# Kernel tuning notes

Measured on AMD Instinct MI355X. Metric: run time of the kernel, lower is better.

The kernel has to match this reference:

```python
import jax, jax.numpy as jnp
import numpy as np

N_NODES = 100000
N_EDGES = 1600000
NFEAT = 128
NHID = 128
NCLASS = 16
NUM_GRAPHS = 64
EPS = 1e-5


def layer_norm(x, g, b):
    mu = jnp.mean(x, axis=-1, keepdims=True)
    var = jnp.mean((x - mu) ** 2, axis=-1, keepdims=True)
    return (x - mu) * jax.lax.rsqrt(var + EPS) * g + b


def gcn_conv(x, W, b, src, dst, ew, n_nodes):
    # PyG GCNConv: h = x @ W^T; add self loops (weight 1); sym-normalize; scatter-add; + bias
    h = x @ W.T                                   # [N, out]
    loop = jnp.arange(n_nodes, dtype=src.dtype)
    src2 = jnp.concatenate([src, loop])
    dst2 = jnp.concatenate([dst, loop])
    ew2 = jnp.concatenate([ew, jnp.ones((n_nodes,), dtype=ew.dtype)])
    deg = jax.ops.segment_sum(ew2, dst2, num_segments=n_nodes)
    dinv = jnp.where(deg > 0, jax.lax.rsqrt(jnp.where(deg > 0, deg, 1.0)), 0.0)
    norm = dinv[src2] * ew2 * dinv[dst2]          # [E+N]
    msg = h[src2] * norm[:, None]                 # gather + scale
    agg = jax.ops.segment_sum(msg, dst2, num_segments=n_nodes)
    return agg + b


def setup_inputs() -> dict:
    key = jax.random.key(0)
    ks = jax.random.split(key, 12)
    kaiming = lambda k, shape: jax.random.normal(k, shape, dtype=jnp.float32) * np.sqrt(2.0 / shape[1])
    ln = lambda k, d: (1.0 + 0.02 * jax.random.normal(k, (d,), dtype=jnp.float32),
                       0.02 * jax.random.normal(jax.random.fold_in(k, 1), (d,), dtype=jnp.float32))
    ln0_g, ln0_b = ln(ks[0], NFEAT)
    ln1_g, ln1_b = ln(ks[1], NHID)
    ln2_g, ln2_b = ln(ks[2], NHID)
    # batch vector: sorted graph ids so each graph is a contiguous node block
    batch = jnp.sort(jax.random.randint(ks[3], (N_NODES,), 0, NUM_GRAPHS)).astype(jnp.int64)
    return {
        "x": jax.random.normal(ks[4], (N_NODES, NFEAT), dtype=jnp.float32),
        "edge_index": jax.random.randint(ks[5], (2, N_EDGES), 0, N_NODES).astype(jnp.int64),
        "batch": batch,
        "edge_weight": jnp.ones((N_EDGES,), dtype=jnp.float32),
        "ln0_g": ln0_g, "ln0_b": ln0_b,
        "W1": kaiming(ks[6], (NHID, NFEAT)), "b1": jnp.zeros((NHID,), jnp.float32),
        "ln1_g": ln1_g, "ln1_b": ln1_b,
        "W2": kaiming(ks[7], (NHID, NHID)), "b2": jnp.zeros((NHID,), jnp.float32),
        "ln2_g": ln2_g, "ln2_b": ln2_b,
        "Wc": kaiming(ks[8], (NCLASS, NHID)), "bc": jnp.zeros((NCLASS,), jnp.float32),
    }


def reference(x, edge_index, batch, edge_weight,
              ln0_g, ln0_b, W1, b1, ln1_g, ln1_b,
              W2, b2, ln2_g, ln2_b, Wc, bc):
    src, dst = edge_index[0], edge_index[1]
    h = layer_norm(x, ln0_g, ln0_b)                       # layer_norm_first
    h = gcn_conv(h, W1, b1, src, dst, edge_weight, N_NODES)
    h = jax.nn.relu(layer_norm(h, ln1_g, ln1_b))          # dropout is identity in eval
    h = gcn_conv(h, W2, b2, src, dst, edge_weight, N_NODES)
    h = jax.nn.relu(layer_norm(h, ln2_g, ln2_b))
    pooled = jax.ops.segment_sum(h, batch, num_segments=NUM_GRAPHS)  # global_add_pool
    logits = pooled @ Wc.T + bc
    return jax.nn.log_softmax(logits, axis=1)
```

## Files before the change

### kernel.cpp

```cpp
#include <hip/hip_runtime.h>
#include <hip/hip_bf16.h>
#include <math.h>

#define N_NODES 100000
#define NFEAT 128
#define NCLASS 16
#define NUM_GRAPHS 64
#define LN_EPS 1e-5f
#define PAD 40
#define BSHIFT 7
#define NBKT 782
#define BCAP 2560
#define EPB 4096

typedef unsigned int uint;
typedef unsigned short ushort;
typedef unsigned char uchar;
typedef short bf16x8 __attribute__((ext_vector_type(8)));
typedef float f32x4 __attribute__((ext_vector_type(4)));
typedef float f32x2 __attribute__((ext_vector_type(2)));

__device__ __forceinline__ float wave_sum64(float v) {
#pragma unroll
    for (int m = 32; m >= 1; m >>= 1) v += __shfl_xor(v, m, 64);
    return v;
}

__device__ __forceinline__ float bf_lo(uint u) { return __uint_as_float(u << 16); }
__device__ __forceinline__ float bf_hi(uint u) { return __uint_as_float(u & 0xffff0000u); }
__device__ __forceinline__ ushort f2bf(float f) {
    uint u = __float_as_uint(f);
    uint r = 0x7fffu + ((u >> 16) & 1u);
    return (ushort)((u + r) >> 16);
}
__device__ __forceinline__ uint pack2bf(float x, float y) {
    return ((uint)f2bf(y) << 16) | (uint)f2bf(x);
}
__device__ __forceinline__ uint pk15(float f) {
    uint u = __float_as_uint(f);
    uint r = 0xFFFFu + ((u >> 17) & 1u);
    return (u + r) >> 17;
}
__device__ __forceinline__ float up15(uint w) {
    return __uint_as_float(w << 17);
}

#if __has_builtin(__builtin_amdgcn_cvt_pk_f32_fp8)
__device__ __forceinline__ f32x2 fp8lo(uint u) {
    return __builtin_amdgcn_cvt_pk_f32_fp8((int)u, false);
}
__device__ __forceinline__ f32x2 fp8hi(uint u) {
    return __builtin_amdgcn_cvt_pk_f32_fp8((int)u, true);
}
#else
__device__ __forceinline__ float fp8_one(uint b) {
    uint em = b & 0x7fu;
    float v;
    if (em >= 0x08u) v = __uint_as_float((((em >> 3) + 120u) << 23) | ((em & 7u) << 20));
    else v = (float)em * (1.0f / 512.0f);
    return (b & 0x80u) ? -v : v;
}
__device__ __forceinline__ f32x2 fp8lo(uint u) {
    f32x2 r;
    r[0] = fp8_one(u & 0xffu);
    r[1] = fp8_one((u >> 8) & 0xffu);
    return r;
}
__device__ __forceinline__ f32x2 fp8hi(uint u) { return fp8lo(u >> 16); }
#endif

#if __has_builtin(__builtin_amdgcn_cvt_pk_fp8_f32)
__device__ __forceinline__ uint f2fp8(float f) {
    return (uint)__builtin_amdgcn_cvt_pk_fp8_f32(f, f, 0, false) & 0xffu;
}
#else
__device__ __forceinline__ uint f2fp8(float f) {
    uint u = __float_as_uint(f);
    uint s = (u >> 24) & 0x80u;
    uint mag = u & 0x7fffffffu;
    if (mag >= 0x43E80000u) return s | 0x7Eu;
    if (mag < 0x3C800000u) {
        uint q = (uint)(__uint_as_float(mag) * 512.0f + 0.5f);
        return s | q;
    }
    uint r = 0x7FFFFu + ((mag >> 20) & 1u);
    mag += r;
    uint e = (mag >> 23) - 120u;
    uint m = (mag >> 20) & 7u;
    if (e > 15u) return s | 0x7Eu;
    return s | (e << 3) | m;
}
#endif

__global__ void k_setup(int* __restrict__ gfill, float* __restrict__ pooled,
                        const float* __restrict__ W1, const float* __restrict__ W2,
                        ushort* __restrict__ Wf) {
    int i = blockIdx.x * 256 + threadIdx.x;
    if (i < NBKT) gfill[i] = 0;
    if (i < NUM_GRAPHS * NFEAT) pooled[i] = 0.0f;
    if (i < 2 * NFEAT * NFEAT) {
        int f = i & 16383;
        const float* W = (i < NFEAT * NFEAT) ? W1 : W2;
        int e = f & 7, lane = (f >> 3) & 63, c = (f >> 9) & 3, t = f >> 11;
        int m = lane & 15, q = lane >> 4;
        Wf[i] = f2bf(W[(t * 16 + m) * NFEAT + c * 32 + q * 8 + e]);
    }
}

__global__ __launch_bounds__(256) void k_bin(const int* __restrict__ dst,
                                             const int* __restrict__ src,
                                             const float* __restrict__ ew,
                                             int* __restrict__ gfill,
                                             uint2* __restrict__ binned, int E) {
    __shared__ int lcnt[NBKT];
    __shared__ int lbase[NBKT];
    int t = threadIdx.x;
    int e0 = blockIdx.x * EPB;
    for (int i = t; i < NBKT; i += 256) lcnt[i] = 0;
    __syncthreads();
    int myb[16], myd[16];
#pragma unroll
    for (int i = 0; i < 16; ++i) {
        int e = e0 + i * 256 + t;
        int b = -1, d = 0;
        if (e < E) {
            d = dst[e];
            b = d >> BSHIFT;
            atomicAdd(&lcnt[b], 1);
        }
        myb[i] = b;
        myd[i] = d;
    }
    __syncthreads();
    for (int i = t; i < NBKT; i += 256) {
        int c = lcnt[i];
        lbase[i] = (c > 0) ? atomicAdd(&gfill[i], c) : 0;
        lcnt[i] = 0;
    }
    __syncthreads();
#pragma unroll
    for (int i = 0; i < 16; ++i) {
        int e = e0 + i * 256 + t;
        if (e >= E) continue;
        int b = myb[i];
        int ofs = lbase[b] + atomicAdd(&lcnt[b], 1);
        if (ofs < BCAP) {
            uint s = (uint)src[e];
            binned[(size_t)b * BCAP + ofs] =
                make_uint2(((uint)(myd[i] & 127) << 17) | s, __float_as_uint(ew[e]));
        }
    }
}

__global__ __launch_bounds__(256) void k_build(const uint2* __restrict__ binned,
                                               const int* __restrict__ gfill,
                                               uint* __restrict__ rowcsr,
                                               int* __restrict__ cnt,
                                               float* __restrict__ dinv, int n) {
    __shared__ uint lcsr[128 * 41];
    __shared__ int lc[128];
    int b = blockIdx.x, t = threadIdx.x;
    int node0 = b << BSHIFT;
    for (int i = t; i < 128 * 41; i += 256) lcsr[i] = 0;
    if (t < 128) lc[t] = 0;
    __syncthreads();
    int c = gfill[b];
    if (c > BCAP) c = BCAP;
    const uint2* rec = binned + (size_t)b * BCAP;
    for (int i = t; i < c; i += 256) {
        uint2 r = rec[i];
        int nl = (int)(r.x >> 17);
        int slot = atomicAdd(&lc[nl], 1);
        if (slot < PAD)
            lcsr[nl * 41 + slot] = ((r.x & 0x1FFFFu) << 15) | pk15(__uint_as_float(r.y));
    }
    __syncthreads();
    int nvalid = n - node0;
    if (nvalid > 128) nvalid = 128;
    if (nvalid <= 0) return;
    size_t gbase = (size_t)node0 * PAD;
    int wtot = nvalid * PAD;
    for (int i = t; i < wtot; i += 256) {
        int nl = i / PAD, sl = i - nl * PAD;
        rowcsr[gbase + i] = lcsr[nl * 41 + sl];
    }
    if (t < nvalid) {
        int cc = lc[t];
        if (cc > PAD) cc = PAD;
        float s = 0.0f;
        for (int r = 0; r < cc; ++r) s += up15(lcsr[t * 41 + r]);
        cnt[node0 + t] = cc;
        dinv[node0 + t] = rsqrtf(1.0f + s);
    }
}

__global__ __launch_bounds__(256) void k_gemm_ln0(const float* __restrict__ X,
                                                  const ushort* __restrict__ Wf,
                                                  const float* __restrict__ dinv,
                                                  const float* __restrict__ lg,
                                                  const float* __restrict__ lb,
                                                  uchar* __restrict__ C, int nrows) {
    int tid = threadIdx.x;
    int wave = tid >> 6, lane = tid & 63;
    int row0 = blockIdx.x * 64 + wave * 16;
    int m = lane & 15, q = lane >> 4;
    int ra = row0 + m;
    float xv[32];
    if (ra < nrows) {
#pragma unroll
        for (int c = 0; c < 4; ++c) {
            float4 p0 = *(const float4*)(X + (size_t)ra * NFEAT + c * 32 + q * 8);
            float4 p1 = *(const float4*)(X + (size_t)ra * NFEAT + c * 32 + q * 8 + 4);
            xv[c * 8 + 0] = p0.x; xv[c * 8 + 1] = p0.y; xv[c * 8 + 2] = p0.z; xv[c * 8 + 3] = p0.w;
            xv[c * 8 + 4] = p1.x; xv[c * 8 + 5] = p1.y; xv[c * 8 + 6] = p1.z; xv[c * 8 + 7] = p1.w;
        }
    } else {
#pragma unroll
        for (int i = 0; i < 32; ++i) xv[i] = 0.0f;
    }
    float s = 0.0f;
#pragma unroll
    for (int i = 0; i < 32; ++i) s += xv[i];
    s += __shfl_xor(s, 16, 64);
    s += __shfl_xor(s, 32, 64);
    float mean = s * (1.0f / NFEAT);
    float v = 0.0f;
#pragma unroll
    for (int i = 0; i < 32; ++i) { float d = xv[i] - mean; v += d * d; }
    v += __shfl_xor(v, 16, 64);
    v += __shfl_xor(v, 32, 64);
    float rs = rsqrtf(v * (1.0f / NFEAT) + LN_EPS);

    bf16x8 a[4];
#pragma unroll
    for (int c = 0; c < 4; ++c) {
        float4 g0 = *(const float4*)(lg + c * 32 + q * 8);
        float4 g1 = *(const float4*)(lg + c * 32 + q * 8 + 4);
        float4 b0 = *(const float4*)(lb + c * 32 + q * 8);
        float4 b1 = *(const float4*)(lb + c * 32 + q * 8 + 4);
        float gv[8] = {g0.x, g0.y, g0.z, g0.w, g1.x, g1.y, g1.z, g1.w};
        float bv[8] = {b0.x, b0.y, b0.z, b0.w, b1.x, b1.y, b1.z, b1.w};
        uint tmp[4];
#pragma unroll
        for (int t2 = 0; t2 < 4; ++t2) {
            float e0 = (xv[c * 8 + 2 * t2] - mean) * rs * gv[2 * t2] + bv[2 * t2];
            float e1 = (xv[c * 8 + 2 * t2 + 1] - mean) * rs * gv[2 * t2 + 1] + bv[2 * t2 + 1];
            tmp[t2] = pack2bf(e0, e1);
        }
        a[c] = *(bf16x8*)tmp;
    }

    int orow[4];
    float sd[4];
#pragma unroll
    for (int r = 0; r < 4; ++r) {
        orow[r] = row0 + q * 4 + r;
        sd[r] = (orow[r] < nrows) ? dinv[orow[r]] : 0.0f;
    }
#pragma unroll
    for (int t = 0; t < 8; ++t) {
        const ushort* bp = Wf + ((t * 4 * 64 + lane) << 3);
        f32x4 acc = {0.0f, 0.0f, 0.0f, 0.0f};
        acc = __builtin_amdgcn_mfma_f32_16x16x32_bf16(a[0], *(const bf16x8*)(bp), acc, 0, 0, 0);
        acc = __builtin_amdgcn_mfma_f32_16x16x32_bf16(a[1], *(const bf16x8*)(bp + 512), acc, 0, 0, 0);
        acc = __builtin_amdgcn_mfma_f32_16x16x32_bf16(a[2], *(const bf16x8*)(bp + 1024), acc, 0, 0, 0);
        acc = __builtin_amdgcn_mfma_f32_16x16x32_bf16(a[3], *(const bf16x8*)(bp + 1536), acc, 0, 0, 0);
#pragma unroll
        for (int r = 0; r < 4; ++r) {
            if (orow[r] < nrows)
                C[(size_t)orow[r] * NFEAT + t * 16 + m] = (uchar)f2fp8(acc[r] * sd[r]);
        }
    }
}

__global__ __launch_bounds__(256) void k_gemm_mfma(const ushort* __restrict__ A,
                                                   const ushort* __restrict__ Wf,
                                                   const float* __restrict__ dinv,
                                                   uchar* __restrict__ C, int nrows) {
    int tid = threadIdx.x;
    int wave = tid >> 6, lane = tid & 63;
    int row0 = blockIdx.x * 64 + wave * 16;
    int m = lane & 15, q = lane >> 4;
    int ra = row0 + m;
    bf16x8 a0 = {0,0,0,0,0,0,0,0}, a1 = a0, a2 = a0, a3 = a0;
    if (ra < nrows) {
        const ushort* p = A + (size_t)ra * NFEAT + q * 8;
        a0 = *(const bf16x8*)(p);
        a1 = *(const bf16x8*)(p + 32);
        a2 = *(const bf16x8*)(p + 64);
        a3 = *(const bf16x8*)(p + 96);
    }
    int orow[4];
    float sd[4];
#pragma unroll
    for (int r = 0; r < 4; ++r) {
        orow[r] = row0 + q * 4 + r;
        sd[r] = (orow[r] < nrows) ? dinv[orow[r]] : 0.0f;
    }
#pragma unroll
    for (int t = 0; t < 8; ++t) {
        const ushort* bp = Wf + ((t * 4 * 64 + lane) << 3);
        f32x4 acc = {0.0f, 0.0f, 0.0f, 0.0f};
        acc = __builtin_amdgcn_mfma_f32_16x16x32_bf16(a0, *(const bf16x8*)(bp), acc, 0, 0, 0);
        acc = __builtin_amdgcn_mfma_f32_16x16x32_bf16(a1, *(const bf16x8*)(bp + 512), acc, 0, 0, 0);
        acc = __builtin_amdgcn_mfma_f32_16x16x32_bf16(a2, *(const bf16x8*)(bp + 1024), acc, 0, 0, 0);
        acc = __builtin_amdgcn_mfma_f32_16x16x32_bf16(a3, *(const bf16x8*)(bp + 1536), acc, 0, 0, 0);
#pragma unroll
        for (int r = 0; r < 4; ++r) {
            if (orow[r] < nrows)
                C[(size_t)orow[r] * NFEAT + t * 16 + m] = (uchar)f2fp8(acc[r] * sd[r]);
        }
    }
}

__global__ __launch_bounds__(256) void k_agg_ln(const uchar* __restrict__ T,
                                                const uint* __restrict__ rowcsr,
                                                const int* __restrict__ cnt,
                                                const float* __restrict__ dinv,
                                                const float* __restrict__ bias,
                                                const float* __restrict__ lng,
                                                const float* __restrict__ lnb,
                                                ushort* __restrict__ out, int n) {
    int wid = blockIdx.x * 4 + (threadIdx.x >> 6);
    int lane = threadIdx.x & 63;
    int half = lane >> 5;
    int l32 = lane & 31;
    int node = wid * 2 + half;
    bool valid = node < n;
    int nodec = valid ? node : 0;

    const uint* Tw = (const uint*)T;
    int c = 0;
    float di = 0.0f;
    if (valid) {
        c = cnt[node];
        di = dinv[node];
    }
    if (c > PAD) c = PAD;
    uint su = Tw[(size_t)nodec * 32 + l32];
    f32x2 s01 = fp8lo(su), s23 = fp8hi(su);
    float a0 = s01[0], a1 = s01[1], a2 = s23[0], a3 = s23[1];

    int cother = __shfl_xor(c, 32, 64);
    int cmax = (c > cother) ? c : cother;
    int rc = (cmax + 7) & ~7;
    const uint* mp = rowcsr + (size_t)nodec * PAD;

    int j = 0;
    for (; j + 16 <= rc; j += 16) {
        uint mw[16];
#pragma unroll
        for (int k = 0; k < 16; k += 4) {
            uint4 m0 = *(const uint4*)(mp + j + k);
            mw[k] = m0.x; mw[k + 1] = m0.y; mw[k + 2] = m0.z; mw[k + 3] = m0.w;
        }
        uint uu[16];
#pragma unroll
        for (int k = 0; k < 16; ++k)
            uu[k] = Tw[(size_t)(mw[k] >> 15) * 32 + l32];
#pragma unroll
        for (int k = 0; k < 16; ++k) {
            float w = up15(mw[k]);
            f32x2 v01 = fp8lo(uu[k]);
            f32x2 v23 = fp8hi(uu[k]);
            a0 = fmaf(v01[0], w, a0);
            a1 = fmaf(v01[1], w, a1);
            a2 = fmaf(v23[0], w, a2);
            a3 = fmaf(v23[1], w, a3);
        }
    }
    for (; j < rc; j += 8) {
        uint4 m0 = *(const uint4*)(mp + j);
        uint4 m1 = *(const uint4*)(mp + j + 4);
        uint mw[8];
        mw[0] = m0.x; mw[1] = m0.y; mw[2] = m0.z; mw[3] = m0.w;
        mw[4] = m1.x; mw[5] = m1.y; mw[6] = m1.z; mw[7] = m1.w;
        uint uu[8];
#pragma unroll
        for (int k = 0; k < 8; ++k)
            uu[k] = Tw[(size_t)(mw[k] >> 15) * 32 + l32];
#pragma unroll
        for (int k = 0; k < 8; ++k) {
            float w = up15(mw[k]);
            f32x2 v01 = fp8lo(uu[k]);
            f32x2 v23 = fp8hi(uu[k]);
            a0 = fmaf(v01[0], w, a0);
            a1 = fmaf(v01[1], w, a1);
            a2 = fmaf(v23[0], w, a2);
            a3 = fmaf(v23[1], w, a3);
        }
    }

    float4 bb = *(const float4*)(bias + 4 * l32);
    float p0 = fmaf(di, a0, bb.x);
    float p1 = fmaf(di, a1, bb.y);
    float p2 = fmaf(di, a2, bb.z);
    float p3 = fmaf(di, a3, bb.w);
    float s = p0 + p1 + p2 + p3;
#pragma unroll
    for (int m = 16; m >= 1; m >>= 1) s += __shfl_xor(s, m, 64);
    float mean = s * (1.0f / NFEAT);
    float d0 = p0 - mean, d1 = p1 - mean, d2 = p2 - mean, d3 = p3 - mean;
    float v = d0 * d0 + d1 * d1 + d2 * d2 + d3 * d3;
#pragma unroll
    for (int m = 16; m >= 1; m >>= 1) v += __shfl_xor(v, m, 64);
    float rs = rsqrtf(v * (1.0f / NFEAT) + LN_EPS);
    float4 gg = *(const float4*)(lng + 4 * l32);
    float4 lbv = *(const float4*)(lnb + 4 * l32);
    float o0 = fmaxf(d0 * rs * gg.x + lbv.x, 0.0f);
    float o1 = fmaxf(d1 * rs * gg.y + lbv.y, 0.0f);
    float o2 = fmaxf(d2 * rs * gg.z + lbv.z, 0.0f);
    float o3 = fmaxf(d3 * rs * gg.w + lbv.w, 0.0f);
    if (valid) {
        uint w0 = pack2bf(o0, o1);
        uint w1 = pack2bf(o2, o3);
        *(uint2*)(out + (size_t)node * NFEAT + 4 * l32) = make_uint2(w0, w1);
    }
}

__global__ __launch_bounds__(256) void k_pool(const ushort* __restrict__ in,
                                              const int* __restrict__ batch,
                                              float* __restrict__ pooled, int n) {
    int wave = blockIdx.x * 4 + (threadIdx.x >> 6);
    int row0 = wave * 16;
    if (row0 >= n) return;
    int lane = threadIdx.x & 63;
    int end = row0 + 16;
    if (end > n) end = n;
    float accx = 0.0f, accy = 0.0f;
    int cur = batch[row0];
    for (int r = row0; r < end; ++r) {
        int g = batch[r];
        if (g != cur) {
            unsafeAtomicAdd(&pooled[cur * NFEAT + 2 * lane], accx);
            unsafeAtomicAdd(&pooled[cur * NFEAT + 2 * lane + 1], accy);
            accx = 0.0f; accy = 0.0f;
            cur = g;
        }
        uint u = *(const uint*)(in + (size_t)r * NFEAT + 2 * lane);
        accx += bf_lo(u);
        accy += bf_hi(u);
    }
    unsafeAtomicAdd(&pooled[cur * NFEAT + 2 * lane], accx);
    unsafeAtomicAdd(&pooled[cur * NFEAT + 2 * lane + 1], accy);
}

__global__ void k_final(const float* __restrict__ pooled, const float* __restrict__ Wc,
                        const float* __restrict__ bc, float* __restrict__ out) {
    __shared__ float p[128];
    __shared__ float lg[NCLASS];
    int g = blockIdx.x, t = threadIdx.x;
    p[t] = pooled[g * 128 + t];
    __syncthreads();
    if (t < NCLASS) {
        float s = bc[t];
        for (int k = 0; k < 128; ++k) s = fmaf(p[k], Wc[t * 128 + k], s);
        lg[t] = s;
    }
    __syncthreads();
    if (t == 0) {
        float m = -1e30f;
        for (int j = 0; j < NCLASS; ++j) m = fmaxf(m, lg[j]);
        float sum = 0.0f;
        for (int j = 0; j < NCLASS; ++j) sum += expf(lg[j] - m);
        float l = logf(sum);
        for (int j = 0; j < NCLASS; ++j) out[g * NCLASS + j] = lg[j] - m - l;
    }
}

extern "C" void kernel_launch(void* const* d_in, const int* in_sizes, int n_in,
                              void* d_out, int out_size, void* d_ws, size_t ws_size,
                              hipStream_t stream) {
    const float* x    = (const float*)d_in[0];
    const int*   ei   = (const int*)d_in[1];
    const int*   batch= (const int*)d_in[2];
    const float* ew   = (const float*)d_in[3];
    const float* ln0g = (const float*)d_in[4];
    const float* ln0b = (const float*)d_in[5];
    const float* W1   = (const float*)d_in[6];
    const float* b1   = (const float*)d_in[7];
    const float* ln1g = (const float*)d_in[8];
    const float* ln1b = (const float*)d_in[9];
    const float* W2   = (const float*)d_in[10];
    const float* b2   = (const float*)d_in[11];
    const float* ln2g = (const float*)d_in[12];
    const float* ln2b = (const float*)d_in[13];
    const float* Wc   = (const float*)d_in[14];
    const float* bc   = (const float*)d_in[15];
    float* out = (float*)d_out;

    int E = in_sizes[1] / 2;
    const int* srcp = ei;
    const int* dstp = ei + E;

    ushort* A     = (ushort*)d_ws;
    ushort* B     = A + (size_t)N_NODES * NFEAT;
    uint*  rowcsr = (uint*)(B + (size_t)N_NODES * NFEAT);
    uint2* binned = (uint2*)(rowcsr + (size_t)N_NODES * PAD);
    float* dinv   = (float*)(binned + (size_t)NBKT * BCAP);
    float* pooled = dinv + N_NODES;
    int*   gfill  = (int*)(pooled + NUM_GRAPHS * NFEAT);
    int*   cnt    = gfill + NBKT;
    ushort* W1f   = (ushort*)(cnt + N_NODES);
    ushort* W2f   = W1f + NFEAT * NFEAT;
    uchar* B8     = (uchar*)B;

    dim3 blk(256);
    int gN = (N_NODES + 255) / 256;
    int gW = ((N_NODES + 1) / 2 + 3) / 4;
    int gG = (N_NODES + 63) / 64;
    int gB = (E + EPB - 1) / EPB;

    k_setup<<<gN, blk, 0, stream>>>(gfill, pooled, W1, W2, W1f);
    k_bin<<<gB, blk, 0, stream>>>(dstp, srcp, ew, gfill, binned, E);
    k_build<<<NBKT, blk, 0, stream>>>(binned, gfill, rowcsr, cnt, dinv, N_NODES);

    k_gemm_ln0<<<gG, blk, 0, stream>>>(x, W1f, dinv, ln0g, ln0b, B8, N_NODES);
    k_agg_ln<<<gW, blk, 0, stream>>>(B8, rowcsr, cnt, dinv, b1, ln1g, ln1b, A, N_NODES);
    k_gemm_mfma<<<gG, blk, 0, stream>>>(A, W2f, dinv, B8, N_NODES);
    k_agg_ln<<<gW, blk, 0, stream>>>(B8, rowcsr, cnt, dinv, b2, ln2g, ln2b, A, N_NODES);
    k_pool<<<(N_NODES + 63) / 64, blk, 0, stream>>>(A, batch, pooled, N_NODES);
    k_final<<<NUM_GRAPHS, dim3(128), 0, stream>>>(pooled, Wc, bc, out);
}
```

Baseline: 292.9 us.

## Build padded CSR directly with global atomics instead of two-pass bucketing

Replaces the bucket-binning plus shared-memory CSR build with a direct scatter. Each edge takes a slot in its destination row through a global atomic counter and writes straight into the zeroed padded row array. A small pass then sums the weights per row for dinv and clamps the counts. This removes the intermediate binned buffer and its extra round trip through memory. In exchange it adds a full zeroing pass over the row array and 1.6M scattered global atomics with uncoalesced writes.

```diff
diff --git a/kernel.cpp b/kernel.cpp
--- a/kernel.cpp
+++ b/kernel.cpp
@@ -8,10 +8,6 @@
 #define NUM_GRAPHS 64
 #define LN_EPS 1e-5f
 #define PAD 40
-#define BSHIFT 7
-#define NBKT 782
-#define BCAP 2560
-#define EPB 4096
 
 typedef unsigned int uint;
 typedef unsigned short ushort;
@@ -19,12 +15,6 @@
 typedef short bf16x8 __attribute__((ext_vector_type(8)));
 typedef float f32x4 __attribute__((ext_vector_type(4)));
 typedef float f32x2 __attribute__((ext_vector_type(2)));
-
-__device__ __forceinline__ float wave_sum64(float v) {
-#pragma unroll
-    for (int m = 32; m >= 1; m >>= 1) v += __shfl_xor(v, m, 64);
-    return v;
-}
 
 __device__ __forceinline__ float bf_lo(uint u) { return __uint_as_float(u << 16); }
 __device__ __forceinline__ float bf_hi(uint u) { return __uint_as_float(u & 0xffff0000u); }
@@ -92,11 +82,15 @@
 }
 #endif
 
-__global__ void k_setup(int* __restrict__ gfill, float* __restrict__ pooled,
-                        const float* __restrict__ W1, const float* __restrict__ W2,
-                        ushort* __restrict__ Wf) {
+__global__ __launch_bounds__(256) void k_zero(uint4* __restrict__ rowcsr4,
+                                              int* __restrict__ cnt,
+                                              float* __restrict__ pooled,
+                                              const float* __restrict__ W1,
+                                              const float* __restrict__ W2,
+                                              ushort* __restrict__ Wf) {
     int i = blockIdx.x * 256 + threadIdx.x;
-    if (i < NBKT) gfill[i] = 0;
+    if (i < (N_NODES * PAD) / 4) rowcsr4[i] = make_uint4(0, 0, 0, 0);
+    if (i < N_NODES) cnt[i] = 0;
     if (i < NUM_GRAPHS * NFEAT) pooled[i] = 0.0f;
     if (i < 2 * NFEAT * NFEAT) {
         int f = i & 16383;
@@ -107,91 +101,54 @@
     }
 }
 
-__global__ __launch_bounds__(256) void k_bin(const int* __restrict__ dst,
-                                             const int* __restrict__ src,
-                                             const float* __restrict__ ew,
-                                             int* __restrict__ gfill,
-                                             uint2* __restrict__ binned, int E) {
-    __shared__ int lcnt[NBKT];
-    __shared__ int lbase[NBKT];
-    int t = threadIdx.x;
-    int e0 = blockIdx.x * EPB;
-    for (int i = t; i < NBKT; i += 256) lcnt[i] = 0;
-    __syncthreads();
-    int myb[16], myd[16];
-#pragma unroll
-    for (int i = 0; i < 16; ++i) {
-        int e = e0 + i * 256 + t;
-        int b = -1, d = 0;
-        if (e < E) {
-            d = dst[e];
-            b = d >> BSHIFT;
-            atomicAdd(&lcnt[b], 1);
-        }
-        myb[i] = b;
-        myd[i] = d;
-    }
-    __syncthreads();
-    for (int i = t; i < NBKT; i += 256) {
-        int c = lcnt[i];
-        lbase[i] = (c > 0) ? atomicAdd(&gfill[i], c) : 0;
-        lcnt[i] = 0;
-    }
-    __syncthreads();
-#pragma unroll
-    for (int i = 0; i < 16; ++i) {
-        int e = e0 + i * 256 + t;
-        if (e >= E) continue;
-        int b = myb[i];
-        int ofs = lbase[b] + atomicAdd(&lcnt[b], 1);
-        if (ofs < BCAP) {
-            uint s = (uint)src[e];
-            binned[(size_t)b * BCAP + ofs] =
-                make_uint2(((uint)(myd[i] & 127) << 17) | s, __float_as_uint(ew[e]));
-        }
-    }
-}
-
-__global__ __launch_bounds__(256) void k_build(const uint2* __restrict__ binned,
-                                               const int* __restrict__ gfill,
-                                               uint* __restrict__ rowcsr,
-                                               int* __restrict__ cnt,
-                                               float* __restrict__ dinv, int n) {
-    __shared__ uint lcsr[128 * 41];
-    __shared__ int lc[128];
-    int b = blockIdx.x, t = threadIdx.x;
-    int node0 = b << BSHIFT;
-    for (int i = t; i < 128 * 41; i += 256) lcsr[i] = 0;
-    if (t < 128) lc[t] = 0;
-    __syncthreads();
-    int c = gfill[b];
-    if (c > BCAP) c = BCAP;
-    const uint2* rec = binned + (size_t)b * BCAP;
-    for (int i = t; i < c; i += 256) {
-        uint2 r = rec[i];
-        int nl = (int)(r.x >> 17);
-        int slot = atomicAdd(&lc[nl], 1);
-        if (slot < PAD)
-            lcsr[nl * 41 + slot] = ((r.x & 0x1FFFFu) << 15) | pk15(__uint_as_float(r.y));
-    }
-    __syncthreads();
-    int nvalid = n - node0;
-    if (nvalid > 128) nvalid = 128;
-    if (nvalid <= 0) return;
-    size_t gbase = (size_t)node0 * PAD;
-    int wtot = nvalid * PAD;
-    for (int i = t; i < wtot; i += 256) {
-        int nl = i / PAD, sl = i - nl * PAD;
-        rowcsr[gbase + i] = lcsr[nl * 41 + sl];
-    }
-    if (t < nvalid) {
-        int cc = lc[t];
-        if (cc > PAD) cc = PAD;
-        float s = 0.0f;
-        for (int r = 0; r < cc; ++r) s += up15(lcsr[t * 41 + r]);
-        cnt[node0 + t] = cc;
-        dinv[node0 + t] = rsqrtf(1.0f + s);
-    }
+__global__ __launch_bounds__(256) void k_direct(const int* __restrict__ dst,
+                                                const int* __restrict__ src,
+                                                const float* __restrict__ ew,
+                                                int* __restrict__ cnt,
+                                                uint* __restrict__ rowcsr, int E) {
+    int e0 = (blockIdx.x * 256 + threadIdx.x) * 4;
+    if (e0 >= E) return;
+    if (e0 + 4 <= E) {
+        int4 d4 = *(const int4*)(dst + e0);
+        int4 s4 = *(const int4*)(src + e0);
+        float4 w4 = *(const float4*)(ew + e0);
+        int dd[4] = {d4.x, d4.y, d4.z, d4.w};
+        int ss[4] = {s4.x, s4.y, s4.z, s4.w};
+        float ww[4] = {w4.x, w4.y, w4.z, w4.w};
+        int slot[4];
+#pragma unroll
+        for (int k = 0; k < 4; ++k) slot[k] = atomicAdd(&cnt[dd[k]], 1);
+#pragma unroll
+        for (int k = 0; k < 4; ++k) {
+            if (slot[k] < PAD)
+                rowcsr[(size_t)dd[k] * PAD + slot[k]] = ((uint)ss[k] << 15) | pk15(ww[k]);
+        }
+    } else {
+        for (int e = e0; e < E; ++e) {
+            int d = dst[e];
+            int slot = atomicAdd(&cnt[d], 1);
+            if (slot < PAD)
+                rowcsr[(size_t)d * PAD + slot] = ((uint)src[e] << 15) | pk15(ew[e]);
+        }
+    }
+}
+
+__global__ __launch_bounds__(256) void k_fix(const uint* __restrict__ rowcsr,
+                                             int* __restrict__ cnt,
+                                             float* __restrict__ dinv, int n) {
+    int i = blockIdx.x * 256 + threadIdx.x;
+    if (i >= n) return;
+    const uint4* p = (const uint4*)(rowcsr + (size_t)i * PAD);
+    float s = 0.0f;
+#pragma unroll
+    for (int r = 0; r < PAD / 4; ++r) {
+        uint4 v = p[r];
+        s += up15(v.x) + up15(v.y) + up15(v.z) + up15(v.w);
+    }
+    int cc = cnt[i];
+    if (cc > PAD) cnt[i] = PAD;
+    (void)cc;
+    dinv[i] = rsqrtf(1.0f + s);
 }
 
 __global__ __launch_bounds__(256) void k_gemm_ln0(const float* __restrict__ X,
@@ -496,24 +453,23 @@
     ushort* A     = (ushort*)d_ws;
     ushort* B     = A + (size_t)N_NODES * NFEAT;
     uint*  rowcsr = (uint*)(B + (size_t)N_NODES * NFEAT);
-    uint2* binned = (uint2*)(rowcsr + (size_t)N_NODES * PAD);
-    float* dinv   = (float*)(binned + (size_t)NBKT * BCAP);
+    float* dinv   = (float*)(rowcsr + (size_t)N_NODES * PAD);
     float* pooled = dinv + N_NODES;
-    int*   gfill  = (int*)(pooled + NUM_GRAPHS * NFEAT);
-    int*   cnt    = gfill + NBKT;
+    int*   cnt    = (int*)(pooled + NUM_GRAPHS * NFEAT);
     ushort* W1f   = (ushort*)(cnt + N_NODES);
     ushort* W2f   = W1f + NFEAT * NFEAT;
     uchar* B8     = (uchar*)B;
 
     dim3 blk(256);
+    int gZ = (N_NODES * PAD / 4 + 255) / 256;
+    int gD = (E + 1023) / 1024;
     int gN = (N_NODES + 255) / 256;
     int gW = ((N_NODES + 1) / 2 + 3) / 4;
     int gG = (N_NODES + 63) / 64;
-    int gB = (E + EPB - 1) / EPB;
-
-    k_setup<<<gN, blk, 0, stream>>>(gfill, pooled, W1, W2, W1f);
-    k_bin<<<gB, blk, 0, stream>>>(dstp, srcp, ew, gfill, binned, E);
-    k_build<<<NBKT, blk, 0, stream>>>(binned, gfill, rowcsr, cnt, dinv, N_NODES);
+
+    k_zero<<<gZ, blk, 0, stream>>>((uint4*)rowcsr, cnt, pooled, W1, W2, W1f);
+    k_direct<<<gD, blk, 0, stream>>>(dstp, srcp, ew, cnt, rowcsr, E);
+    k_fix<<<gN, blk, 0, stream>>>(rowcsr, cnt, dinv, N_NODES);
 
     k_gemm_ln0<<<gG, blk, 0, stream>>>(x, W1f, dinv, ln0g, ln0b, B8, N_NODES);
     k_agg_ln<<<gW, blk, 0, stream>>>(B8, rowcsr, cnt, dinv, b1, ln1g, ln1b, A, N_NODES);
```

After: 389.0 us. 32.8% more time.

## Replace global-atomic bucket fill with per-block local sort and offset table

Applied to the files above, without the earlier changes.

k_bin now computes a block-local prefix sum over bucket counts, sorts its edge records into shared memory, writes them contiguously, and stores a per-block ushort offset table, instead of reserving slots via global atomics on gfill. k_build then walks each input block's slice for its bucket, with threads striding over blocks. This removes global atomics and the gfill zeroing, and it writes records coalesced instead of scattering them. In exchange k_build does many small serial per-thread loops with scattered reads across 391 block slices, which may load-balance poorly.

```diff
diff --git a/kernel.cpp b/kernel.cpp
--- a/kernel.cpp
+++ b/kernel.cpp
@@ -10,8 +10,9 @@
 #define PAD 40
 #define BSHIFT 7
 #define NBKT 782
-#define BCAP 2560
 #define EPB 4096
+#define NBLKMAX 400
+#define LSTRIDE 784
 
 typedef unsigned int uint;
 typedef unsigned short ushort;
@@ -19,12 +20,6 @@
 typedef short bf16x8 __attribute__((ext_vector_type(8)));
 typedef float f32x4 __attribute__((ext_vector_type(4)));
 typedef float f32x2 __attribute__((ext_vector_type(2)));
-
-__device__ __forceinline__ float wave_sum64(float v) {
-#pragma unroll
-    for (int m = 32; m >= 1; m >>= 1) v += __shfl_xor(v, m, 64);
-    return v;
-}
 
 __device__ __forceinline__ float bf_lo(uint u) { return __uint_as_float(u << 16); }
 __device__ __forceinline__ float bf_hi(uint u) { return __uint_as_float(u & 0xffff0000u); }
@@ -92,11 +87,11 @@
 }
 #endif
 
-__global__ void k_setup(int* __restrict__ gfill, float* __restrict__ pooled,
-                        const float* __restrict__ W1, const float* __restrict__ W2,
-                        ushort* __restrict__ Wf) {
+__global__ __launch_bounds__(256) void k_setup(float* __restrict__ pooled,
+                                               const float* __restrict__ W1,
+                                               const float* __restrict__ W2,
+                                               ushort* __restrict__ Wf) {
     int i = blockIdx.x * 256 + threadIdx.x;
-    if (i < NBKT) gfill[i] = 0;
     if (i < NUM_GRAPHS * NFEAT) pooled[i] = 0.0f;
     if (i < 2 * NFEAT * NFEAT) {
         int f = i & 16383;
@@ -110,12 +105,15 @@
 __global__ __launch_bounds__(256) void k_bin(const int* __restrict__ dst,
                                              const int* __restrict__ src,
                                              const float* __restrict__ ew,
-                                             int* __restrict__ gfill,
-                                             uint2* __restrict__ binned, int E) {
-    __shared__ int lcnt[NBKT];
-    __shared__ int lbase[NBKT];
+                                             uint2* __restrict__ binned,
+                                             ushort* __restrict__ lofsG, int E) {
+    __shared__ uint lcnt[NBKT];
+    __shared__ uint ofsarr[NBKT + 1];
+    __shared__ uint wsum[4];
+    __shared__ uint2 srec[EPB];
     int t = threadIdx.x;
-    int e0 = blockIdx.x * EPB;
+    int blk = blockIdx.x;
+    int e0 = blk * EPB;
     for (int i = t; i < NBKT; i += 256) lcnt[i] = 0;
     __syncthreads();
     int myb[16], myd[16];
@@ -126,37 +124,67 @@
         if (e < E) {
             d = dst[e];
             b = d >> BSHIFT;
-            atomicAdd(&lcnt[b], 1);
+            atomicAdd(&lcnt[b], 1u);
         }
         myb[i] = b;
         myd[i] = d;
     }
     __syncthreads();
-    for (int i = t; i < NBKT; i += 256) {
-        int c = lcnt[i];
-        lbase[i] = (c > 0) ? atomicAdd(&gfill[i], c) : 0;
-        lcnt[i] = 0;
-    }
+    int lane = t & 63, wv = t >> 6;
+    uint v[4];
+    uint s = 0;
+    int b0 = t * 4;
+#pragma unroll
+    for (int k = 0; k < 4; ++k) {
+        int ix = b0 + k;
+        v[k] = (ix < NBKT) ? lcnt[ix] : 0u;
+        s += v[k];
+    }
+    uint inc = s;
+#pragma unroll
+    for (int o = 1; o < 64; o <<= 1) {
+        uint nn = __shfl_up(inc, o, 64);
+        if (lane >= o) inc += nn;
+    }
+    if (lane == 63) wsum[wv] = inc;
+    __syncthreads();
+    uint wbase = 0;
+    for (int k = 0; k < wv; ++k) wbase += wsum[k];
+    uint excl = wbase + inc - s;
+#pragma unroll
+    for (int k = 0; k < 4; ++k) {
+        int ix = b0 + k;
+        if (ix < NBKT) {
+            ofsarr[ix] = excl;
+            excl += v[k];
+        }
+    }
+    if (t == 0) ofsarr[NBKT] = wsum[0] + wsum[1] + wsum[2] + wsum[3];
+    __syncthreads();
+    for (int i = t; i <= NBKT; i += 256) lofsG[(size_t)blk * LSTRIDE + i] = (ushort)ofsarr[i];
+    for (int i = t; i < NBKT; i += 256) lcnt[i] = 0;
     __syncthreads();
 #pragma unroll
     for (int i = 0; i < 16; ++i) {
+        int b = myb[i];
+        if (b < 0) continue;
         int e = e0 + i * 256 + t;
-        if (e >= E) continue;
-        int b = myb[i];
-        int ofs = lbase[b] + atomicAdd(&lcnt[b], 1);
-        if (ofs < BCAP) {
-            uint s = (uint)src[e];
-            binned[(size_t)b * BCAP + ofs] =
-                make_uint2(((uint)(myd[i] & 127) << 17) | s, __float_as_uint(ew[e]));
-        }
-    }
+        uint pos = ofsarr[b] + atomicAdd(&lcnt[b], 1u);
+        srec[pos] = make_uint2(((uint)(myd[i] & 127) << 17) | (uint)src[e],
+                               __float_as_uint(ew[e]));
+    }
+    __syncthreads();
+    const uint4* sp = (const uint4*)srec;
+    uint4* gp = (uint4*)(binned + (size_t)blk * EPB);
+    for (int i = t; i < EPB / 2; i += 256) gp[i] = sp[i];
 }
 
 __global__ __launch_bounds__(256) void k_build(const uint2* __restrict__ binned,
-                                               const int* __restrict__ gfill,
+                                               const ushort* __restrict__ lofsG,
                                                uint* __restrict__ rowcsr,
                                                int* __restrict__ cnt,
-                                               float* __restrict__ dinv, int n) {
+                                               float* __restrict__ dinv,
+                                               int nblk, int n) {
     __shared__ uint lcsr[128 * 41];
     __shared__ int lc[128];
     int b = blockIdx.x, t = threadIdx.x;
@@ -164,15 +192,17 @@
     for (int i = t; i < 128 * 41; i += 256) lcsr[i] = 0;
     if (t < 128) lc[t] = 0;
     __syncthreads();
-    int c = gfill[b];
-    if (c > BCAP) c = BCAP;
-    const uint2* rec = binned + (size_t)b * BCAP;
-    for (int i = t; i < c; i += 256) {
-        uint2 r = rec[i];
-        int nl = (int)(r.x >> 17);
-        int slot = atomicAdd(&lc[nl], 1);
-        if (slot < PAD)
-            lcsr[nl * 41 + slot] = ((r.x & 0x1FFFFu) << 15) | pk15(__uint_as_float(r.y));
+    for (int blk = t; blk < nblk; blk += 256) {
+        const ushort* lp = lofsG + (size_t)blk * LSTRIDE + b;
+        int s = lp[0], e2 = lp[1];
+        const uint2* rp = binned + (size_t)blk * EPB;
+        for (int i = s; i < e2; ++i) {
+            uint2 r = rp[i];
+            int nl = (int)(r.x >> 17);
+            int slot = atomicAdd(&lc[nl], 1);
+            if (slot < PAD)
+                lcsr[nl * 41 + slot] = ((r.x & 0x1FFFFu) << 15) | pk15(__uint_as_float(r.y));
+        }
     }
     __syncthreads();
     int nvalid = n - node0;
@@ -497,23 +527,23 @@
     ushort* B     = A + (size_t)N_NODES * NFEAT;
     uint*  rowcsr = (uint*)(B + (size_t)N_NODES * NFEAT);
     uint2* binned = (uint2*)(rowcsr + (size_t)N_NODES * PAD);
-    float* dinv   = (float*)(binned + (size_t)NBKT * BCAP);
+    ushort* lofsG = (ushort*)(binned + (size_t)NBLKMAX * EPB);
+    float* dinv   = (float*)(lofsG + (size_t)NBLKMAX * LSTRIDE);
     float* pooled = dinv + N_NODES;
-    int*   gfill  = (int*)(pooled + NUM_GRAPHS * NFEAT);
-    int*   cnt    = gfill + NBKT;
+    int*   cnt    = (int*)(pooled + NUM_GRAPHS * NFEAT);
     ushort* W1f   = (ushort*)(cnt + N_NODES);
     ushort* W2f   = W1f + NFEAT * NFEAT;
     uchar* B8     = (uchar*)B;
 
     dim3 blk(256);
-    int gN = (N_NODES + 255) / 256;
+    int gS = (2 * NFEAT * NFEAT + 255) / 256;
+    int gB = (E + EPB - 1) / EPB;
     int gW = ((N_NODES + 1) / 2 + 3) / 4;
     int gG = (N_NODES + 63) / 64;
-    int gB = (E + EPB - 1) / EPB;
-
-    k_setup<<<gN, blk, 0, stream>>>(gfill, pooled, W1, W2, W1f);
-    k_bin<<<gB, blk, 0, stream>>>(dstp, srcp, ew, gfill, binned, E);
-    k_build<<<NBKT, blk, 0, stream>>>(binned, gfill, rowcsr, cnt, dinv, N_NODES);
+
+    k_setup<<<gS, blk, 0, stream>>>(pooled, W1, W2, W1f);
+    k_bin<<<gB, blk, 0, stream>>>(dstp, srcp, ew, binned, lofsG, E);
+    k_build<<<NBKT, blk, 0, stream>>>(binned, lofsG, rowcsr, cnt, dinv, gB, N_NODES);
 
     k_gemm_ln0<<<gG, blk, 0, stream>>>(x, W1f, dinv, ln0g, ln0b, B8, N_NODES);
     k_agg_ln<<<gW, blk, 0, stream>>>(B8, rowcsr, cnt, dinv, b1, ln1g, ln1b, A, N_NODES);
```

Result: faster. 286.8 us (-2.1%).
